# Performance work log

Measured on AMD Instinct MI355X. Metric: run time of the kernel, lower is better.

Reference implementation:

```python
import jax, jax.numpy as jnp
import numpy as np

B, H, W, CIN, COUT = 16, 256, 256, 64, 64
M1, M2 = 32, 32  # retained Fourier modes; M2 <= W//2+1


def setup_inputs() -> dict:
    key = jax.random.key(0)
    k0, k1, k2, k3, k4 = jax.random.split(key, 5)
    # complex_scale = sqrt(2/(Cin+Cout)) / sqrt(2), per module default init
    cscale = (2.0 / (CIN + COUT)) ** 0.5 / 2.0 ** 0.5
    x = jax.random.normal(k0, (B, H, W, CIN), jnp.float32)
    wshape = (CIN, COUT, M1, M2)
    w1_re = cscale * jax.random.normal(k1, wshape, jnp.float32)
    w1_im = cscale * jax.random.normal(k2, wshape, jnp.float32)
    w2_re = cscale * jax.random.normal(k3, wshape, jnp.float32)
    w2_im = cscale * jax.random.normal(k4, wshape, jnp.float32)
    bias = jnp.zeros((COUT,), jnp.float32)
    return {"x": x, "w1_re": w1_re, "w1_im": w1_im,
            "w2_re": w2_re, "w2_im": w2_im, "bias": bias}


def reference(x, w1_re, w1_im, w2_re, w2_im, bias):
    # x: (B,H,W,Cin) -> rfft over spatial axes, norm='forward'
    x_ft = jnp.fft.rfftn(x, axes=(1, 2), norm='forward')  # (B,H,W//2+1,Cin) c64
    w1 = jax.lax.complex(w1_re, w1_im)  # (Cin,Cout,M1,M2)
    w2 = jax.lax.complex(w2_re, w2_im)
    # two corners: low-positive and low-negative frequencies along axis 1
    top = jnp.einsum('bxyi,ioxy->bxyo', x_ft[:, :M1, :M2, :], w1)
    bot = jnp.einsum('bxyi,ioxy->bxyo', x_ft[:, -M1:, :M2, :], w2)
    out_ft = jnp.zeros((B, H, W // 2 + 1, COUT), dtype=jnp.complex64)
    out_ft = out_ft.at[:, :M1, :M2, :].set(top)
    out_ft = out_ft.at[:, -M1:, :M2, :].set(bot)
    out = jnp.fft.irfftn(out_ft, s=(H, W), axes=(1, 2), norm='forward')
    return out + bias.reshape(1, 1, 1, COUT)
```

## Files before the change

### kernel.cpp

```cpp
#include <hip/hip_runtime.h>
#include <math.h>

#define NB 16
#define NH 256
#define NW 256
#define TWO_PI 6.28318530717958647692f
#define FSCALE (1.0f/65536.0f)

#define OFF_X  ((size_t)1 << 24)
#define OFF_OF (((size_t)1 << 24) + ((size_t)1 << 22))
#define WS_FLOATS_NEEDED (((size_t)1 << 24) + ((size_t)2 << 22))

typedef __attribute__((ext_vector_type(8))) short short8;
typedef __attribute__((ext_vector_type(4))) float f32x4;

__device__ __forceinline__ unsigned short f2bf(float f) {
    unsigned int u = __float_as_uint(f);
    unsigned int r = (u + 0x7FFFu + ((u >> 16) & 1u)) >> 16;
    return (unsigned short)r;
}

#define XPITCH 264
__global__ __launch_bounds__(256) void k1_dft_w(const float* __restrict__ x,
                                                float* __restrict__ WS) {
    __shared__ float2 tw[256];
    __shared__ unsigned short Al[64 * XPITCH];
    __shared__ unsigned short Xl[64 * XPITCH];
    int t = threadIdx.x;
    { float s, c; sincosf(TWO_PI * (float)t * (1.0f/256.0f), &s, &c);
      tw[t] = make_float2(c, s); }
    __syncthreads();
    {
        int m  = t >> 2;
        int w0 = (t & 3) * 64;
        int ky = m & 31;
        for (int dw8 = 0; dw8 < 8; ++dw8) {
            short8 v8;
#pragma unroll
            for (int j = 0; j < 8; ++j) {
                int w = w0 + dw8*8 + j;
                float2 cs = tw[(ky * w) & 255];
                float v = (m < 32) ? cs.x : -cs.y;
                v8[j] = (short)f2bf(v * FSCALE);
            }
            *(short8*)&Al[m * XPITCH + w0 + dw8*8] = v8;
        }
    }
    int wave = t >> 6, lane = t & 63;
    int col = lane & 15, kq = lane >> 4;
    for (int u = 0; u < 4; ++u) {
        int bh = blockIdx.x * 4 + u;
        __syncthreads();
        {
            const float* xs = x + (size_t)bh * 16384 + t * 64;
            for (int i4 = 0; i4 < 16; ++i4) {
                float4 v = *(const float4*)(xs + i4*4);
                Xl[(i4*4+0)*XPITCH + t] = f2bf(v.x);
                Xl[(i4*4+1)*XPITCH + t] = f2bf(v.y);
                Xl[(i4*4+2)*XPITCH + t] = f2bf(v.z);
                Xl[(i4*4+3)*XPITCH + t] = f2bf(v.w);
            }
        }
        __syncthreads();
        f32x4 acc[4];
#pragma unroll
        for (int n = 0; n < 4; ++n) acc[n] = (f32x4){0.f, 0.f, 0.f, 0.f};
#pragma unroll
        for (int kk = 0; kk < 8; ++kk) {
            int k = kk*32 + kq*8;
            short8 af = *(const short8*)&Al[(wave*16 + col) * XPITCH + k];
#pragma unroll
            for (int n = 0; n < 4; ++n) {
                short8 bf = *(const short8*)&Xl[(n*16 + col) * XPITCH + k];
                acc[n] = __builtin_amdgcn_mfma_f32_16x16x32_bf16(af, bf, acc[n], 0, 0, 0);
            }
        }
        int comp = wave >> 1;
        int kyb  = (wave & 1) * 16;
        float* gp = WS + (size_t)bh * 4096 + comp * 2048;
#pragma unroll
        for (int n = 0; n < 4; ++n)
#pragma unroll
            for (int q = 0; q < 4; ++q) {
                int ky = kyb + kq*4 + q;
                gp[ky*64 + n*16 + col] = acc[n][q];
            }
    }
}

#define K2P 264
__global__ __launch_bounds__(1024) void k2_dft_h(float* __restrict__ WS) {
    int b  = blockIdx.x >> 5;
    int ky = blockIdx.x & 31;
    int t  = threadIdx.x;
    __shared__ float2 tw[256];
    __shared__ unsigned short A2l[64 * K2P];
    __shared__ unsigned short B1l[64 * K2P];
    __shared__ unsigned short B2l[64 * K2P];
    if (t < 256) { float s, c; sincosf(TWO_PI * (float)t * (1.0f/256.0f), &s, &c);
                   tw[t] = make_float2(c, s); }
    __syncthreads();
    {
        int r = t >> 4, s0 = (t & 15) * 16;
        int kxe = (r < 32) ? r : r + 192;
#pragma unroll
        for (int c8 = 0; c8 < 2; ++c8) {
            short8 v8;
#pragma unroll
            for (int j = 0; j < 8; ++j) {
                int s = s0 + c8*8 + j;
                float v = (s <= 128) ? tw[(kxe * s) & 255].x
                                     : tw[(kxe * (s - 128)) & 255].y;
                v8[j] = (short)f2bf(v);
            }
            *(short8*)&A2l[r*K2P + s0 + c8*8] = v8;
        }
    }
    int i = t & 63, hg = t >> 6;
    const float* gre = WS + (size_t)(b*256)*4096 + ky*64 + i;
    for (int s2 = 0; hg + 16*s2 <= 128; ++s2) {
        int hp = hg + 16*s2;
        float are = gre[(size_t)hp*4096];
        float aim = gre[(size_t)hp*4096 + 2048];
        if (hp == 0 || hp == 128) {
            B1l[i*K2P + hp] = f2bf(are);
            B2l[i*K2P + hp] = f2bf(aim);
        } else {
            float bre = gre[(size_t)(256-hp)*4096];
            float bim = gre[(size_t)(256-hp)*4096 + 2048];
            B1l[i*K2P + hp]       = f2bf(are + bre);
            B1l[i*K2P + 128 + hp] = f2bf(aim - bim);
            B2l[i*K2P + hp]       = f2bf(aim + bim);
            B2l[i*K2P + 128 + hp] = f2bf(bre - are);
        }
    }
    __syncthreads();
    int wave = t >> 6, col = t & 15, kq = (t >> 4) & 3;
    int mt = wave >> 2, n = wave & 3;
    f32x4 ar = (f32x4){0.f,0.f,0.f,0.f}, ai = (f32x4){0.f,0.f,0.f,0.f};
#pragma unroll
    for (int kk = 0; kk < 8; ++kk) {
        int k = kk*32 + kq*8;
        short8 af = *(const short8*)&A2l[(mt*16 + col)*K2P + k];
        short8 b1 = *(const short8*)&B1l[(n*16 + col)*K2P + k];
        short8 b2 = *(const short8*)&B2l[(n*16 + col)*K2P + k];
        ar = __builtin_amdgcn_mfma_f32_16x16x32_bf16(af, b1, ar, 0, 0, 0);
        ai = __builtin_amdgcn_mfma_f32_16x16x32_bf16(af, b2, ai, 0, 0, 0);
    }
#pragma unroll
    for (int q = 0; q < 4; ++q) {
        int kxrow = mt*16 + kq*4 + q;
        float* dst = WS + OFF_X + (((size_t)b*64 + kxrow)*32 + ky)*128
                        + 2*(n*16 + col);
        *(float2*)dst = make_float2(ar[q], ai[q]);
    }
}

__global__ __launch_bounds__(512) void k3_mix(const float* __restrict__ w1re,
                                              const float* __restrict__ w1im,
                                              const float* __restrict__ w2re,
                                              const float* __restrict__ w2im,
                                              float* __restrict__ WS) {
    int kx  = blockIdx.x & 63;
    int kyq = blockIdx.x >> 6;
    int t   = threadIdx.x;
    __shared__ float2 lx[8192];
    __shared__ float  lw[2][2][4][576];
    const float* wre = (kx < 32) ? w1re : w2re;
    const float* wim = (kx < 32) ? w1im : w2im;
    int m = kx & 31;
    for (int n = t; n < 8192; n += 512) {
        int bb = n >> 9, ky8 = (n >> 6) & 7, ii = n & 63;
        lx[n] = *(const float2*)(WS + OFF_X
                 + (((size_t)bb*64 + kx)*32 + kyq*8 + ky8)*128 + 2*ii);
    }
    int sarr = t & 1, so = (t >> 1) & 63, si4 = t >> 7;
    const float* wsrc = sarr ? wim : wre;
    size_t sbase = (size_t)m*32 + kyq*8;
    int kyl = t >> 6;
    int o   = t & 63;
    int kyg = kyq*8 + kyl;
    float ar[16], ai[16];
#pragma unroll
    for (int bb = 0; bb < 16; ++bb) { ar[bb] = 0.f; ai[bb] = 0.f; }

    float4 wa, wb;
    {
        const float* src = wsrc + ((size_t)(si4*64 + so)*1024 + sbase);
        wa = *(const float4*)src; wb = *(const float4*)(src + 4);
        float* dst = &lw[0][sarr][si4][so*9];
        dst[0]=wa.x; dst[1]=wa.y; dst[2]=wa.z; dst[3]=wa.w;
        dst[4]=wb.x; dst[5]=wb.y; dst[6]=wb.z; dst[7]=wb.w;
    }
    __syncthreads();

    for (int k = 0; k < 16; ++k) {
        int i0 = k*4;
        float4 na, nb;
        if (k < 15) {
            const float* src = wsrc + ((size_t)((i0+4+si4)*64 + so)*1024 + sbase);
            na = *(const float4*)src; nb = *(const float4*)(src + 4);
        }
#pragma unroll
        for (int di = 0; di < 4; ++di) {
            float wr = lw[k & 1][0][di][o*9 + kyl];
            float wi = lw[k & 1][1][di][o*9 + kyl];
            int ii = i0 + di;
#pragma unroll
            for (int bb = 0; bb < 16; ++bb) {
                float2 xv = lx[(bb*8 + kyl)*64 + ii];
                ar[bb] = fmaf(xv.x, wr, fmaf(-xv.y, wi, ar[bb]));
                ai[bb] = fmaf(xv.x, wi, fmaf( xv.y, wr, ai[bb]));
            }
        }
        if (k < 15) {
            float* dst = &lw[(k+1) & 1][sarr][si4][so*9];
            dst[0]=na.x; dst[1]=na.y; dst[2]=na.z; dst[3]=na.w;
            dst[4]=nb.x; dst[5]=nb.y; dst[6]=nb.z; dst[7]=nb.w;
        }
        __syncthreads();
    }
#pragma unroll
    for (int bb = 0; bb < 16; ++bb) {
        float* cp = WS + OFF_OF + (((size_t)bb*64 + kx)*32 + kyg)*128 + 2*o;
        *(float2*)cp = make_float2(ar[bb], ai[bb]);
    }
}

#define K4P 136
__global__ __launch_bounds__(1024) void k4_idft_h(float* __restrict__ WS) {
    int b  = blockIdx.x >> 5;
    int ky = blockIdx.x & 31;
    int t  = threadIdx.x;
    __shared__ float2 tw[256];
    __shared__ unsigned short A4l[256 * K4P];
    __shared__ unsigned short B1l[64 * K4P];
    __shared__ unsigned short B2l[64 * K4P];
    if (t < 256) { float s, c; sincosf(TWO_PI * (float)t * (1.0f/256.0f), &s, &c);
                   tw[t] = make_float2(c, s); }
    __syncthreads();
    {
        int h = t >> 2, s0 = (t & 3) * 32;
#pragma unroll
        for (int c8 = 0; c8 < 4; ++c8) {
            short8 v8;
#pragma unroll
            for (int j = 0; j < 8; ++j) {
                int s = s0 + c8*8 + j;
                int ds = s & 63;
                int kxe = (ds < 32) ? ds : ds + 192;
                float2 cs = tw[(kxe * h) & 255];
                v8[j] = (short)f2bf((s < 64) ? cs.x : cs.y);
            }
            *(short8*)&A4l[h*K4P + s0 + c8*8] = v8;
        }
    }
    int o = t & 63, kg = t >> 6;
#pragma unroll
    for (int s = 0; s < 4; ++s) {
        int kx = kg*4 + s;
        float2 v = *(const float2*)(WS + OFF_OF
                    + (((size_t)b*64 + kx)*32 + ky)*128 + 2*o);
        B1l[o*K4P + kx]      = f2bf(v.x);
        B1l[o*K4P + 64 + kx] = f2bf(-v.y);
        B2l[o*K4P + kx]      = f2bf(v.y);
        B2l[o*K4P + 64 + kx] = f2bf(v.x);
    }
    __syncthreads();
    int wave = t >> 6, col = t & 15, kq = (t >> 4) & 3;
#pragma unroll
    for (int e = 0; e < 4; ++e) {
        int p = wave*4 + e, mt = p >> 2, n = p & 3;
        f32x4 ar = (f32x4){0.f,0.f,0.f,0.f}, ai = (f32x4){0.f,0.f,0.f,0.f};
#pragma unroll
        for (int kk = 0; kk < 4; ++kk) {
            int k = kk*32 + kq*8;
            short8 af = *(const short8*)&A4l[(mt*16 + col)*K4P + k];
            short8 b1 = *(const short8*)&B1l[(n*16 + col)*K4P + k];
            short8 b2 = *(const short8*)&B2l[(n*16 + col)*K4P + k];
            ar = __builtin_amdgcn_mfma_f32_16x16x32_bf16(af, b1, ar, 0, 0, 0);
            ai = __builtin_amdgcn_mfma_f32_16x16x32_bf16(af, b2, ai, 0, 0, 0);
        }
#pragma unroll
        for (int q = 0; q < 4; ++q) {
            int h  = mt*16 + kq*4 + q;
            int o2 = n*16 + col;
            float* dp = WS + (size_t)(b*256 + h)*4096 + (ky*64 + o2)*2;
            *(float2*)dp = make_float2(ar[q], ai[q]);
        }
    }
}

#define APITCH 72
__global__ __launch_bounds__(256) void k5_idft_w(const float* __restrict__ bias,
                                                 const float* __restrict__ WS,
                                                 float* __restrict__ out) {
    int t = threadIdx.x;
    __shared__ float2 tw[256];
    __shared__ unsigned short T5[256 * APITCH];
    __shared__ unsigned short Bl[64 * APITCH];
    { float s, c; sincosf(TWO_PI * (float)t * (1.0f/256.0f), &s, &c);
      tw[t] = make_float2(c, s); }
    __syncthreads();
    {
        int w = t;
#pragma unroll
        for (int ky = 0; ky < 32; ++ky) {
            float2 cs = tw[(ky * w) & 255];
            float sc = ky ? 2.f : 1.f;
            T5[w*APITCH + ky]      = f2bf(sc * cs.x);
            T5[w*APITCH + 32 + ky] = f2bf(-sc * cs.y);
        }
    }
    int o = t & 63, kg = t >> 6;
    int wave = t >> 6, col = t & 15, kq = (t >> 4) & 3;
    float bv[4];
#pragma unroll
    for (int n = 0; n < 4; ++n) bv[n] = bias[n*16 + col];

    for (int u = 0; u < 4; ++u) {
        int bh = blockIdx.x * 4 + u;
        __syncthreads();
        {
            const float* tp = WS + (size_t)bh * 4096;
#pragma unroll
            for (int kk = 0; kk < 8; ++kk) {
                int ky = kg*8 + kk;
                float2 v = *(const float2*)(tp + (ky*64 + o)*2);
                Bl[o*APITCH + ky]      = f2bf(v.x);
                Bl[o*APITCH + 32 + ky] = f2bf(v.y);
            }
        }
        __syncthreads();
        f32x4 acc[4][4];
#pragma unroll
        for (int mt = 0; mt < 4; ++mt)
#pragma unroll
            for (int n = 0; n < 4; ++n) acc[mt][n] = (f32x4){0.f,0.f,0.f,0.f};
#pragma unroll
        for (int kk = 0; kk < 2; ++kk) {
            short8 af[4];
#pragma unroll
            for (int mt = 0; mt < 4; ++mt)
                af[mt] = *(const short8*)&T5[(wave*64 + mt*16 + col)*APITCH
                                             + kk*32 + kq*8];
#pragma unroll
            for (int n = 0; n < 4; ++n) {
                short8 bf = *(const short8*)&Bl[(n*16 + col)*APITCH
                                                + kk*32 + kq*8];
#pragma unroll
                for (int mt = 0; mt < 4; ++mt)
                    acc[mt][n] = __builtin_amdgcn_mfma_f32_16x16x32_bf16(
                                     af[mt], bf, acc[mt][n], 0, 0, 0);
            }
        }
        float* R = out + (size_t)bh * 16384;
#pragma unroll
        for (int mt = 0; mt < 4; ++mt)
#pragma unroll
            for (int n = 0; n < 4; ++n)
#pragma unroll
                for (int q = 0; q < 4; ++q) {
                    int w = wave*64 + mt*16 + kq*4 + q;
                    R[w*64 + n*16 + col] = acc[mt][n][q] + bv[n];
                }
    }
}

extern "C" void kernel_launch(void* const* d_in, const int* in_sizes, int n_in,
                              void* d_out, int out_size, void* d_ws, size_t ws_size,
                              hipStream_t stream) {
    (void)in_sizes; (void)n_in; (void)out_size;
    if (ws_size < WS_FLOATS_NEEDED * sizeof(float)) return;
    const float* x    = (const float*)d_in[0];
    const float* w1re = (const float*)d_in[1];
    const float* w1im = (const float*)d_in[2];
    const float* w2re = (const float*)d_in[3];
    const float* w2im = (const float*)d_in[4];
    const float* bias = (const float*)d_in[5];
    float* O  = (float*)d_out;
    float* WS = (float*)d_ws;

    k1_dft_w <<<1024,  256, 0, stream>>>(x, WS);
    k2_dft_h <<< 512, 1024, 0, stream>>>(WS);
    k3_mix   <<< 256,  512, 0, stream>>>(w1re, w1im, w2re, w2im, WS);
    k4_idft_h<<< 512, 1024, 0, stream>>>(WS);
    k5_idft_w<<<1024,  256, 0, stream>>>(bias, WS, O);
}
```

Before: 232.3 us.

## Store all inter-stage workspace buffers as packed bf16 complex pairs

```diff
diff --git a/kernel.cpp b/kernel.cpp
--- a/kernel.cpp
+++ b/kernel.cpp
@@ -7,9 +7,9 @@
 #define TWO_PI 6.28318530717958647692f
 #define FSCALE (1.0f/65536.0f)
 
-#define OFF_X  ((size_t)1 << 24)
-#define OFF_OF (((size_t)1 << 24) + ((size_t)1 << 22))
-#define WS_FLOATS_NEEDED (((size_t)1 << 24) + ((size_t)2 << 22))
+#define OFF_X  ((size_t)1 << 23)
+#define OFF_OF (((size_t)1 << 23) + ((size_t)1 << 21))
+#define WS_FLOATS_NEEDED (((size_t)1 << 23) + ((size_t)2 << 21))
 
 typedef __attribute__((ext_vector_type(8))) short short8;
 typedef __attribute__((ext_vector_type(4))) float f32x4;
@@ -18,6 +18,12 @@
     unsigned int u = __float_as_uint(f);
     unsigned int r = (u + 0x7FFFu + ((u >> 16) & 1u)) >> 16;
     return (unsigned short)r;
+}
+__device__ __forceinline__ float bf2f(unsigned int u16) {
+    return __uint_as_float(u16 << 16);
+}
+__device__ __forceinline__ unsigned int pk2(float a, float b) {
+    return (unsigned int)f2bf(a) | ((unsigned int)f2bf(b) << 16);
 }
 
 #define XPITCH 264
@@ -48,6 +54,7 @@
     }
     int wave = t >> 6, lane = t & 63;
     int col = lane & 15, kq = lane >> 4;
+    unsigned int* Gu = (unsigned int*)WS;
     for (int u = 0; u < 4; ++u) {
         int bh = blockIdx.x * 4 + u;
         __syncthreads();
@@ -68,23 +75,25 @@
 #pragma unroll
         for (int kk = 0; kk < 8; ++kk) {
             int k = kk*32 + kq*8;
-            short8 af = *(const short8*)&Al[(wave*16 + col) * XPITCH + k];
+            short8 af = *(const short8*)&Xl[(wave*16 + col) * XPITCH + k];
 #pragma unroll
             for (int n = 0; n < 4; ++n) {
-                short8 bf = *(const short8*)&Xl[(n*16 + col) * XPITCH + k];
+                short8 bf = *(const short8*)&Al[(n*16 + col) * XPITCH + k];
                 acc[n] = __builtin_amdgcn_mfma_f32_16x16x32_bf16(af, bf, acc[n], 0, 0, 0);
             }
         }
-        int comp = wave >> 1;
-        int kyb  = (wave & 1) * 16;
-        float* gp = WS + (size_t)bh * 4096 + comp * 2048;
-#pragma unroll
-        for (int n = 0; n < 4; ++n)
-#pragma unroll
-            for (int q = 0; q < 4; ++q) {
-                int ky = kyb + kq*4 + q;
-                gp[ky*64 + n*16 + col] = acc[n][q];
-            }
+        int i0 = wave*16 + kq*4;
+        unsigned int* gp = Gu + (size_t)bh * 2048;
+#pragma unroll
+        for (int g = 0; g < 2; ++g) {
+            int ky = g*16 + col;
+            uint4 pk;
+            pk.x = pk2(acc[g][0], acc[g+2][0]);
+            pk.y = pk2(acc[g][1], acc[g+2][1]);
+            pk.z = pk2(acc[g][2], acc[g+2][2]);
+            pk.w = pk2(acc[g][3], acc[g+2][3]);
+            *(uint4*)(gp + ky*64 + i0) = pk;
+        }
     }
 }
 
@@ -117,17 +126,18 @@
         }
     }
     int i = t & 63, hg = t >> 6;
-    const float* gre = WS + (size_t)(b*256)*4096 + ky*64 + i;
+    const unsigned int* gu = (const unsigned int*)WS
+                             + (size_t)(b*256)*2048 + ky*64 + i;
     for (int s2 = 0; hg + 16*s2 <= 128; ++s2) {
         int hp = hg + 16*s2;
-        float are = gre[(size_t)hp*4096];
-        float aim = gre[(size_t)hp*4096 + 2048];
+        unsigned int ga = gu[(size_t)hp*2048];
+        float are = bf2f(ga & 0xffffu), aim = bf2f(ga >> 16);
         if (hp == 0 || hp == 128) {
             B1l[i*K2P + hp] = f2bf(are);
             B2l[i*K2P + hp] = f2bf(aim);
         } else {
-            float bre = gre[(size_t)(256-hp)*4096];
-            float bim = gre[(size_t)(256-hp)*4096 + 2048];
+            unsigned int gb = gu[(size_t)(256-hp)*2048];
+            float bre = bf2f(gb & 0xffffu), bim = bf2f(gb >> 16);
             B1l[i*K2P + hp]       = f2bf(are + bre);
             B1l[i*K2P + 128 + hp] = f2bf(aim - bim);
             B2l[i*K2P + hp]       = f2bf(aim + bim);
@@ -147,12 +157,11 @@
         ar = __builtin_amdgcn_mfma_f32_16x16x32_bf16(af, b1, ar, 0, 0, 0);
         ai = __builtin_amdgcn_mfma_f32_16x16x32_bf16(af, b2, ai, 0, 0, 0);
     }
+    unsigned int* Xu = (unsigned int*)(WS + OFF_X);
 #pragma unroll
     for (int q = 0; q < 4; ++q) {
         int kxrow = mt*16 + kq*4 + q;
-        float* dst = WS + OFF_X + (((size_t)b*64 + kxrow)*32 + ky)*128
-                        + 2*(n*16 + col);
-        *(float2*)dst = make_float2(ar[q], ai[q]);
+        Xu[(((size_t)b*64 + kxrow)*32 + ky)*64 + n*16 + col] = pk2(ar[q], ai[q]);
     }
 }
 
@@ -169,10 +178,11 @@
     const float* wre = (kx < 32) ? w1re : w2re;
     const float* wim = (kx < 32) ? w1im : w2im;
     int m = kx & 31;
+    const unsigned int* Xu = (const unsigned int*)(WS + OFF_X);
     for (int n = t; n < 8192; n += 512) {
         int bb = n >> 9, ky8 = (n >> 6) & 7, ii = n & 63;
-        lx[n] = *(const float2*)(WS + OFF_X
-                 + (((size_t)bb*64 + kx)*32 + kyq*8 + ky8)*128 + 2*ii);
+        unsigned int g = Xu[(((size_t)bb*64 + kx)*32 + kyq*8 + ky8)*64 + ii];
+        lx[n] = make_float2(bf2f(g & 0xffffu), bf2f(g >> 16));
     }
     int sarr = t & 1, so = (t >> 1) & 63, si4 = t >> 7;
     const float* wsrc = sarr ? wim : wre;
@@ -220,10 +230,10 @@
         }
         __syncthreads();
     }
+    unsigned int* ofu = (unsigned int*)(WS + OFF_OF);
 #pragma unroll
     for (int bb = 0; bb < 16; ++bb) {
-        float* cp = WS + OFF_OF + (((size_t)bb*64 + kx)*32 + kyg)*128 + 2*o;
-        *(float2*)cp = make_float2(ar[bb], ai[bb]);
+        ofu[(((size_t)bb*64 + kx)*32 + kyg)*64 + o] = pk2(ar[bb], ai[bb]);
     }
 }
 
@@ -256,18 +266,21 @@
         }
     }
     int o = t & 63, kg = t >> 6;
+    const unsigned int* ofu = (const unsigned int*)(WS + OFF_OF);
 #pragma unroll
     for (int s = 0; s < 4; ++s) {
         int kx = kg*4 + s;
-        float2 v = *(const float2*)(WS + OFF_OF
-                    + (((size_t)b*64 + kx)*32 + ky)*128 + 2*o);
-        B1l[o*K4P + kx]      = f2bf(v.x);
-        B1l[o*K4P + 64 + kx] = f2bf(-v.y);
-        B2l[o*K4P + kx]      = f2bf(v.y);
-        B2l[o*K4P + 64 + kx] = f2bf(v.x);
+        unsigned int g = ofu[(((size_t)b*64 + kx)*32 + ky)*64 + o];
+        unsigned short lo = (unsigned short)(g & 0xffffu);
+        unsigned short hi = (unsigned short)(g >> 16);
+        B1l[o*K4P + kx]      = lo;
+        B1l[o*K4P + 64 + kx] = hi ^ 0x8000u;
+        B2l[o*K4P + kx]      = hi;
+        B2l[o*K4P + 64 + kx] = lo;
     }
     __syncthreads();
     int wave = t >> 6, col = t & 15, kq = (t >> 4) & 3;
+    unsigned int* tmpu = (unsigned int*)WS;
 #pragma unroll
     for (int e = 0; e < 4; ++e) {
         int p = wave*4 + e, mt = p >> 2, n = p & 3;
@@ -285,8 +298,7 @@
         for (int q = 0; q < 4; ++q) {
             int h  = mt*16 + kq*4 + q;
             int o2 = n*16 + col;
-            float* dp = WS + (size_t)(b*256 + h)*4096 + (ky*64 + o2)*2;
-            *(float2*)dp = make_float2(ar[q], ai[q]);
+            tmpu[(size_t)(b*256 + h)*2048 + ky*64 + o2] = pk2(ar[q], ai[q]);
         }
     }
 }
@@ -322,13 +334,13 @@
         int bh = blockIdx.x * 4 + u;
         __syncthreads();
         {
-            const float* tp = WS + (size_t)bh * 4096;
+            const unsigned int* tpu = (const unsigned int*)WS + (size_t)bh * 2048;
 #pragma unroll
             for (int kk = 0; kk < 8; ++kk) {
                 int ky = kg*8 + kk;
-                float2 v = *(const float2*)(tp + (ky*64 + o)*2);
-                Bl[o*APITCH + ky]      = f2bf(v.x);
-                Bl[o*APITCH + 32 + ky] = f2bf(v.y);
+                unsigned int g = tpu[ky*64 + o];
+                Bl[o*APITCH + ky]      = (unsigned short)(g & 0xffffu);
+                Bl[o*APITCH + 32 + ky] = (unsigned short)(g >> 16);
             }
         }
         __syncthreads();
```

Result: faster. 215.5 us (-7.2%).
